# Kernel optimization log

Measured on AMD Instinct MI355X. Metric: run time of the kernel, lower is better.

The kernel has to match this reference:

```python
import jax, jax.numpy as jnp
import numpy as np

BLOCK = 16  # NVFP4 block size (per-block FP8 scale over 16 FP4 values)
FP4_GRID = jnp.array([0.0, 0.5, 1.0, 1.5, 2.0, 3.0, 4.0, 6.0], dtype=jnp.float32)
FP4_MIDS = jnp.array([0.25, 0.75, 1.25, 1.75, 2.5, 3.5, 5.0], dtype=jnp.float32)


def _quantize_fp4(v):
    # round-to-nearest onto the signed E2M1 grid {0,.5,1,1.5,2,3,4,6}
    a = jnp.clip(jnp.abs(v), 0.0, 6.0)
    idx = jnp.searchsorted(FP4_MIDS, a)
    return jnp.sign(v) * FP4_GRID[idx]


def _block_quantize(x):
    # returns (fp4 values, per-16-block scales) such that x ~= q * scale_blocked
    M, K = x.shape
    B = K // BLOCK
    xb = x.reshape(M, B, BLOCK)
    s = jnp.max(jnp.abs(xb), axis=-1) / 6.0 + 1e-8  # [M, B]
    q = _quantize_fp4(xb / s[:, :, None]).reshape(M, K)
    return q, s


def setup_inputs() -> dict:
    key = jax.random.key(0)
    k1, k2, k3 = jax.random.split(key, 3)
    M, K, N = 8192, 4096, 4096
    bsz, q_len = 4, 2048

    x_raw = jax.random.normal(k1, (M, K), dtype=jnp.float32)
    w_raw = jax.random.normal(k2, (N, K), dtype=jnp.float32) * 0.02

    # global weight scale as in NVFP4_reorder_quantize_w: max(w)/(448*6)
    scale_w_global = jnp.max(w_raw) / (448.0 * 6.0)
    qw, scale_w = _block_quantize(w_raw / scale_w_global)

    # activation global scale (produced upstream by the activation quantizer)
    scale_x_global = jnp.max(x_raw) / (448.0 * 6.0)
    qx, scale_x = _block_quantize(x_raw / scale_x_global)

    bias = jax.random.normal(k3, (N,), dtype=jnp.float32) * 0.01

    return {
        "qx": qx,                      # [M, K] FP4-grid values
        "scale_x": scale_x,            # [M, K//16] block scales
        "scale": scale_x_global,       # scalar global activation scale
        "qw": qw,                      # [N, K] FP4-grid values
        "scale_w": scale_w,            # [N, K//16] block scales
        "scale_w_global": scale_w_global,
        "bias": bias,                  # [N]
        "bsz": bsz,
        "q_len": q_len,
    }


def reference(qx, scale_x, scale, qw, scale_w, scale_w_global, bias, bsz, q_len):
    # Dequant-scaled GEMM: y = (qx .* sx)(qw .* sw)^T * (scale * scale_w_global) + bias
    M, K = qx.shape
    N = qw.shape[0]
    B = K // BLOCK
    xd = (qx.reshape(M, B, BLOCK) * scale_x[:, :, None]).reshape(M, K)
    wd = (qw.reshape(N, B, BLOCK) * scale_w[:, :, None]).reshape(N, K)
    y = jnp.einsum("mk,nk->mn", xd, wd) * (scale * scale_w_global)
    y = y + bias
    return y.reshape(bsz, q_len, -1)
```

## Files before the change

kernel.cpp:

```cpp
#include <hip/hip_runtime.h>
#include <cstdint>

#define K_DIM 4096
#define ROWB 13
#define NU   (K_DIM / 32)

typedef __bf16 bf16x8 __attribute__((ext_vector_type(8)));
typedef float f32x4 __attribute__((ext_vector_type(4)));

__device__ inline unsigned short f2bf(float f) {
    union { float f; unsigned int u; } v; v.f = f;
    unsigned int u = v.u;
    return (unsigned short)((u + 0x7FFFu + ((u >> 16) & 1u)) >> 16);
}

__device__ __forceinline__ void gload16(const void* g, void* l) {
    __builtin_amdgcn_global_load_lds(
        (const __attribute__((address_space(1))) unsigned int*)g,
        (__attribute__((address_space(3))) unsigned int*)l,
        16, 0, 0);
}

__global__ __launch_bounds__(256) void dequant2_kernel(
        const float* __restrict__ qx, const float* __restrict__ sx,
        unsigned short* __restrict__ xd, long t8x,
        const float* __restrict__ qw, const float* __restrict__ sw,
        unsigned short* __restrict__ wd, long t8w) {
    long i = (long)blockIdx.x * blockDim.x + threadIdx.x;
    if (i >= t8x + t8w) return;
    const float* q; const float* s; unsigned short* o;
    if (i < t8x) { q = qx; s = sx; o = xd; }
    else         { q = qw; s = sw; o = wd; i -= t8x; }
    long e = i * 8;
    float sc = s[e >> 4];
    float4 v0 = *(const float4*)(q + e);
    float4 v1 = *(const float4*)(q + e + 4);
    union { unsigned short h[8]; uint4 u; } ov;
    ov.h[0] = f2bf(v0.x * sc); ov.h[1] = f2bf(v0.y * sc);
    ov.h[2] = f2bf(v0.z * sc); ov.h[3] = f2bf(v0.w * sc);
    ov.h[4] = f2bf(v1.x * sc); ov.h[5] = f2bf(v1.y * sc);
    ov.h[6] = f2bf(v1.z * sc); ov.h[7] = f2bf(v1.w * sc);
    *(uint4*)(o + e) = ov.u;
}


__global__ __launch_bounds__(512, 2) void gemm256_kernel(
        const unsigned short* __restrict__ A,
        const unsigned short* __restrict__ B,
        const float* __restrict__ sg1, const float* __restrict__ sg2,
        const float* __restrict__ bias,
        float* __restrict__ out, int M, int N) {
    __shared__ __align__(16) char lds[131072];

    const int tid  = threadIdx.x;
    const int lane = tid & 63;
    const int wid  = tid >> 6;
    const int wm   = wid >> 2;
    const int wn   = wid & 3;
    const int l15  = lane & 15;
    const int cb   = (lane >> 4) << 4;
    const int scb  = ((lane & 3) ^ ((lane >> 3) & 3)) << 4;

    const int nbn = N >> 8;
    const int nwg = (M >> 8) * nbn;
    const int cpx = nwg >> 3;
    const int bid = blockIdx.x;
    const int swz = (bid & 7) * cpx + (bid >> 3);
    const int tile_m = (swz / nbn) << 8;
    const int tile_n = (swz % nbn) << 8;

    const int grow = lane >> 2;
    const char* gA0 = (const char*)A +
        ((size_t)(tile_m + 32 * wid + grow) << ROWB) + scb;
    const char* gA1 = gA0 + ((size_t)16 << ROWB);
    const char* gB0 = (const char*)B +
        ((size_t)(tile_n + 32 * wid + grow) << ROWB) + scb;
    const char* gB1 = gB0 + ((size_t)16 << ROWB);
    const int dA0 = wid * 2048;
    const int dB0 = 16384 + wid * 2048;

    const int arow = wm * 128 + l15;
    const int aoff = arow * 64 + (cb ^ (((arow >> 1) & 3) << 4));
    const int brow = wn * 64 + l15;
    const int boff = 16384 + brow * 64 + (cb ^ (((brow >> 1) & 3) << 4));

    f32x4 acc[8][4];
#pragma unroll
    for (int mb = 0; mb < 8; ++mb)
#pragma unroll
        for (int nb = 0; nb < 4; ++nb) acc[mb][nb] = (f32x4){0.f, 0.f, 0.f, 0.f};

#pragma unroll
    for (int pu = 0; pu < 3; ++pu) {
        char* Sb = lds + (pu << 15);
        const int kb = pu << 6;
        gload16(gA0 + kb, Sb + dA0);
        gload16(gA1 + kb, Sb + dA0 + 1024);
        gload16(gB0 + kb, Sb + dB0);
        gload16(gB1 + kb, Sb + dB0 + 1024);
    }
    asm volatile("s_waitcnt vmcnt(8)" ::: "memory");
    __builtin_amdgcn_s_barrier();

    for (int ub = 0; ub < NU; ub += 4) {
#pragma unroll
        for (int uu = 0; uu < 4; ++uu) {
            const int u = ub + uu;
            const char* Ab = lds + (uu << 15);
            char* Sb = lds + (((uu + 3) & 3) << 15);
            const int skb = ((u + 3 < NU) ? (u + 3) : (NU - 1)) << 6;

            bf16x8 bfr[4], afr[4];
#pragma unroll
            for (int nb = 0; nb < 4; ++nb)
                bfr[nb] = *(const bf16x8*)(Ab + boff + nb * 1024);
#pragma unroll
            for (int mb = 0; mb < 4; ++mb)
                afr[mb] = *(const bf16x8*)(Ab + aoff + mb * 1024);
            gload16(gA0 + skb, Sb + dA0);
            gload16(gA1 + skb, Sb + dA0 + 1024);
            __builtin_amdgcn_s_barrier();
            __builtin_amdgcn_s_setprio(1);
#pragma unroll
            for (int mb = 0; mb < 4; ++mb)
#pragma unroll
                for (int nb = 0; nb < 4; ++nb)
                    acc[mb][nb] = __builtin_amdgcn_mfma_f32_16x16x32_bf16(
                        afr[mb], bfr[nb], acc[mb][nb], 0, 0, 0);
            __builtin_amdgcn_s_setprio(0);

            bf16x8 afr2[4];
#pragma unroll
            for (int mb = 0; mb < 4; ++mb)
                afr2[mb] = *(const bf16x8*)(Ab + aoff + 4096 + mb * 1024);
            gload16(gB0 + skb, Sb + dB0);
            gload16(gB1 + skb, Sb + dB0 + 1024);
            __builtin_amdgcn_s_barrier();
            __builtin_amdgcn_s_setprio(1);
#pragma unroll
            for (int mb = 0; mb < 4; ++mb)
#pragma unroll
                for (int nb = 0; nb < 4; ++nb)
                    acc[mb + 4][nb] = __builtin_amdgcn_mfma_f32_16x16x32_bf16(
                        afr2[mb], bfr[nb], acc[mb + 4][nb], 0, 0, 0);
            __builtin_amdgcn_s_setprio(0);

            asm volatile("s_waitcnt vmcnt(8)" ::: "memory");
            __builtin_amdgcn_s_barrier();
        }
    }

    const float gs = sg1[0] * sg2[0];
    const int row0 = tile_m + wm * 128 + ((lane >> 4) << 2);
    const int col0 = tile_n + wn * 64 + l15;
    float bv[4];
#pragma unroll
    for (int nb = 0; nb < 4; ++nb) bv[nb] = bias[col0 + nb * 16];
#pragma unroll
    for (int mb = 0; mb < 8; ++mb)
#pragma unroll
        for (int nb = 0; nb < 4; ++nb) {
            const int col = col0 + nb * 16;
#pragma unroll
            for (int j = 0; j < 4; ++j)
                out[(size_t)(row0 + mb * 16 + j) * N + col] =
                    acc[mb][nb][j] * gs + bv[nb];
        }
}

__global__ __launch_bounds__(256) void gemm_fused_kernel(
        const float* __restrict__ qx, const float* __restrict__ sx,
        const float* __restrict__ qw, const float* __restrict__ sw,
        const float* __restrict__ sg1, const float* __restrict__ sg2,
        const float* __restrict__ bias,
        float* __restrict__ out, int M, int N) {
    __shared__ __align__(16) unsigned short As[128 * 32];
    __shared__ __align__(16) unsigned short Bs[128 * 32];
    const int tid  = threadIdx.x;
    const int lane = tid & 63;
    const int wid  = tid >> 6;
    const int tile_n = blockIdx.x * 128;
    const int tile_m = blockIdx.y * 128;
    const int wm = wid >> 1, wn = wid & 1;
    f32x4 acc[16];
#pragma unroll
    for (int i = 0; i < 16; ++i) acc[i] = (f32x4){0.f, 0.f, 0.f, 0.f};
    const int l15 = lane & 15;
    const int lk  = (lane >> 4) * 8;
    for (int kt = 0; kt < K_DIM / 32; ++kt) {
#pragma unroll
        for (int cc = 0; cc < 2; ++cc) {
            const int c   = tid + cc * 256;
            const int row = c >> 2;
            const int col = (c & 3) * 8;
            const int gk  = kt * 32 + col;
            {
                const float* qp = qx + (long)(tile_m + row) * K_DIM + gk;
                float s = sx[(long)(tile_m + row) * (K_DIM / 16) + (gk >> 4)];
                float4 a0 = *(const float4*)qp;
                float4 a1 = *(const float4*)(qp + 4);
                union { unsigned short h[8]; uint4 u; } o;
                o.h[0] = f2bf(a0.x * s); o.h[1] = f2bf(a0.y * s);
                o.h[2] = f2bf(a0.z * s); o.h[3] = f2bf(a0.w * s);
                o.h[4] = f2bf(a1.x * s); o.h[5] = f2bf(a1.y * s);
                o.h[6] = f2bf(a1.z * s); o.h[7] = f2bf(a1.w * s);
                *(uint4*)&As[row * 32 + col] = o.u;
            }
            {
                const float* qp = qw + (long)(tile_n + row) * K_DIM + gk;
                float s = sw[(long)(tile_n + row) * (K_DIM / 16) + (gk >> 4)];
                float4 a0 = *(const float4*)qp;
                float4 a1 = *(const float4*)(qp + 4);
                union { unsigned short h[8]; uint4 u; } o;
                o.h[0] = f2bf(a0.x * s); o.h[1] = f2bf(a0.y * s);
                o.h[2] = f2bf(a0.z * s); o.h[3] = f2bf(a0.w * s);
                o.h[4] = f2bf(a1.x * s); o.h[5] = f2bf(a1.y * s);
                o.h[6] = f2bf(a1.z * s); o.h[7] = f2bf(a1.w * s);
                *(uint4*)&Bs[row * 32 + col] = o.u;
            }
        }
        __syncthreads();
        const unsigned short* pa = As + (wm * 64 + l15) * 32 + lk;
        const unsigned short* pb = Bs + (wn * 64 + l15) * 32 + lk;
        bf16x8 a[4], b[4];
#pragma unroll
        for (int i = 0; i < 4; ++i) {
            a[i] = *(const bf16x8*)(pa + i * 16 * 32);
            b[i] = *(const bf16x8*)(pb + i * 16 * 32);
        }
#pragma unroll
        for (int mi = 0; mi < 4; ++mi)
#pragma unroll
            for (int ni = 0; ni < 4; ++ni)
                acc[mi * 4 + ni] = __builtin_amdgcn_mfma_f32_16x16x32_bf16(
                    a[mi], b[ni], acc[mi * 4 + ni], 0, 0, 0);
        __syncthreads();
    }
    const float gs = sg1[0] * sg2[0];
    const int row0 = tile_m + wm * 64 + (lane >> 4) * 4;
    const int col0 = tile_n + wn * 64 + l15;
#pragma unroll
    for (int mi = 0; mi < 4; ++mi)
#pragma unroll
        for (int ni = 0; ni < 4; ++ni) {
            const int col = col0 + ni * 16;
            const float bv = bias[col];
#pragma unroll
            for (int j = 0; j < 4; ++j)
                out[(long)(row0 + mi * 16 + j) * N + col] =
                    acc[mi * 4 + ni][j] * gs + bv;
        }
}

extern "C" void kernel_launch(void* const* d_in, const int* in_sizes, int n_in,
                              void* d_out, int out_size, void* d_ws, size_t ws_size,
                              hipStream_t stream) {
    const float* qx   = (const float*)d_in[0];
    const float* sx   = (const float*)d_in[1];
    const float* sc   = (const float*)d_in[2];
    const float* qw   = (const float*)d_in[3];
    const float* sw   = (const float*)d_in[4];
    const float* swg  = (const float*)d_in[5];
    const float* bias = (const float*)d_in[6];
    float* out = (float*)d_out;

    const int M = in_sizes[0] / K_DIM;
    const int N = in_sizes[3] / K_DIM;

    const size_t needA = (size_t)M * K_DIM * sizeof(unsigned short);
    const size_t needB = (size_t)N * K_DIM * sizeof(unsigned short);

    if (ws_size >= needA + needB) {
        unsigned short* xd = (unsigned short*)d_ws;
        unsigned short* wd = (unsigned short*)((char*)d_ws + needA);
        long t8x = (long)M * K_DIM / 8;
        long t8w = (long)N * K_DIM / 8;
        long tot = t8x + t8w;
        dequant2_kernel<<<(int)((tot + 255) / 256), 256, 0, stream>>>(
            qx, sx, xd, t8x, qw, sw, wd, t8w);
        const int nwg = (M / 256) * (N / 256);
        gemm256_kernel<<<nwg, 512, 0, stream>>>(xd, wd, sc, swg, bias, out, M, N);
    } else {
        dim3 grid(N / 128, M / 128);
        gemm_fused_kernel<<<grid, 256, 0, stream>>>(
            qx, sx, qw, sw, sc, swg, bias, out, M, N);
    }
}
```

Measured before the change: 283.8 us.

## Switch GEMM inner loop to 32x32x16 bf16 MFMA and drop mid-iteration barriers

```diff
diff --git a/kernel.cpp b/kernel.cpp
--- a/kernel.cpp
+++ b/kernel.cpp
@@ -6,7 +6,8 @@
 #define NU   (K_DIM / 32)
 
 typedef __bf16 bf16x8 __attribute__((ext_vector_type(8)));
-typedef float f32x4 __attribute__((ext_vector_type(4)));
+typedef float f32x4  __attribute__((ext_vector_type(4)));
+typedef float f32x16 __attribute__((ext_vector_type(16)));
 
 __device__ inline unsigned short f2bf(float f) {
     union { float f; unsigned int u; } v; v.f = f;
@@ -57,8 +58,8 @@
     const int wid  = tid >> 6;
     const int wm   = wid >> 2;
     const int wn   = wid & 3;
-    const int l15  = lane & 15;
-    const int cb   = (lane >> 4) << 4;
+    const int l31  = lane & 31;
+    const int lhi  = lane >> 5;
     const int scb  = ((lane & 3) ^ ((lane >> 3) & 3)) << 4;
 
     const int nbn = N >> 8;
@@ -79,16 +80,22 @@
     const int dA0 = wid * 2048;
     const int dB0 = 16384 + wid * 2048;
 
-    const int arow = wm * 128 + l15;
-    const int aoff = arow * 64 + (cb ^ (((arow >> 1) & 3) << 4));
-    const int brow = wn * 64 + l15;
-    const int boff = 16384 + brow * 64 + (cb ^ (((brow >> 1) & 3) << 4));
-
-    f32x4 acc[8][4];
-#pragma unroll
-    for (int mb = 0; mb < 8; ++mb)
-#pragma unroll
-        for (int nb = 0; nb < 4; ++nb) acc[mb][nb] = (f32x4){0.f, 0.f, 0.f, 0.f};
+    const int arow = wm * 128 + l31;
+    const int axv  = (arow >> 1) & 3;
+    const int aok0 = arow * 64 + ((lhi ^ axv) << 4);
+    const int aok1 = arow * 64 + (((2 + lhi) ^ axv) << 4);
+    const int brow = wn * 64 + l31;
+    const int bxv  = (brow >> 1) & 3;
+    const int bok0 = 16384 + brow * 64 + ((lhi ^ bxv) << 4);
+    const int bok1 = 16384 + brow * 64 + (((2 + lhi) ^ bxv) << 4);
+
+    f32x16 acc[4][2];
+#pragma unroll
+    for (int mb = 0; mb < 4; ++mb)
+#pragma unroll
+        for (int nb = 0; nb < 2; ++nb)
+#pragma unroll
+            for (int j = 0; j < 16; ++j) acc[mb][nb][j] = 0.f;
 
 #pragma unroll
     for (int pu = 0; pu < 3; ++pu) {
@@ -105,44 +112,37 @@
     for (int ub = 0; ub < NU; ub += 4) {
 #pragma unroll
         for (int uu = 0; uu < 4; ++uu) {
-            const int u = ub + uu;
-            const char* Ab = lds + (uu << 15);
+            const int u  = ub + uu;
+            const char* Sl = lds + (uu << 15);
             char* Sb = lds + (((uu + 3) & 3) << 15);
             const int skb = ((u + 3 < NU) ? (u + 3) : (NU - 1)) << 6;
 
-            bf16x8 bfr[4], afr[4];
-#pragma unroll
-            for (int nb = 0; nb < 4; ++nb)
-                bfr[nb] = *(const bf16x8*)(Ab + boff + nb * 1024);
-#pragma unroll
-            for (int mb = 0; mb < 4; ++mb)
-                afr[mb] = *(const bf16x8*)(Ab + aoff + mb * 1024);
             gload16(gA0 + skb, Sb + dA0);
             gload16(gA1 + skb, Sb + dA0 + 1024);
-            __builtin_amdgcn_s_barrier();
-            __builtin_amdgcn_s_setprio(1);
-#pragma unroll
-            for (int mb = 0; mb < 4; ++mb)
-#pragma unroll
-                for (int nb = 0; nb < 4; ++nb)
-                    acc[mb][nb] = __builtin_amdgcn_mfma_f32_16x16x32_bf16(
-                        afr[mb], bfr[nb], acc[mb][nb], 0, 0, 0);
-            __builtin_amdgcn_s_setprio(0);
-
-            bf16x8 afr2[4];
-#pragma unroll
-            for (int mb = 0; mb < 4; ++mb)
-                afr2[mb] = *(const bf16x8*)(Ab + aoff + 4096 + mb * 1024);
             gload16(gB0 + skb, Sb + dB0);
             gload16(gB1 + skb, Sb + dB0 + 1024);
-            __builtin_amdgcn_s_barrier();
+
+            bf16x8 af[4][2], bf[2][2];
+#pragma unroll
+            for (int nb = 0; nb < 2; ++nb) {
+                bf[nb][0] = *(const bf16x8*)(Sl + bok0 + nb * 2048);
+                bf[nb][1] = *(const bf16x8*)(Sl + bok1 + nb * 2048);
+            }
+#pragma unroll
+            for (int mb = 0; mb < 4; ++mb) {
+                af[mb][0] = *(const bf16x8*)(Sl + aok0 + mb * 2048);
+                af[mb][1] = *(const bf16x8*)(Sl + aok1 + mb * 2048);
+            }
+
             __builtin_amdgcn_s_setprio(1);
 #pragma unroll
             for (int mb = 0; mb < 4; ++mb)
 #pragma unroll
-                for (int nb = 0; nb < 4; ++nb)
-                    acc[mb + 4][nb] = __builtin_amdgcn_mfma_f32_16x16x32_bf16(
-                        afr2[mb], bfr[nb], acc[mb + 4][nb], 0, 0, 0);
+                for (int nb = 0; nb < 2; ++nb)
+#pragma unroll
+                    for (int ks = 0; ks < 2; ++ks)
+                        acc[mb][nb] = __builtin_amdgcn_mfma_f32_32x32x16_bf16(
+                            af[mb][ks], bf[nb][ks], acc[mb][nb], 0, 0, 0);
             __builtin_amdgcn_s_setprio(0);
 
             asm volatile("s_waitcnt vmcnt(8)" ::: "memory");
@@ -151,20 +151,23 @@
     }
 
     const float gs = sg1[0] * sg2[0];
-    const int row0 = tile_m + wm * 128 + ((lane >> 4) << 2);
-    const int col0 = tile_n + wn * 64 + l15;
-    float bv[4];
-#pragma unroll
-    for (int nb = 0; nb < 4; ++nb) bv[nb] = bias[col0 + nb * 16];
-#pragma unroll
-    for (int mb = 0; mb < 8; ++mb)
-#pragma unroll
-        for (int nb = 0; nb < 4; ++nb) {
-            const int col = col0 + nb * 16;
-#pragma unroll
-            for (int j = 0; j < 4; ++j)
-                out[(size_t)(row0 + mb * 16 + j) * N + col] =
-                    acc[mb][nb][j] * gs + bv[nb];
+    const int row0 = tile_m + wm * 128 + 4 * lhi;
+    const int col0 = tile_n + wn * 64 + l31;
+    float bv[2];
+#pragma unroll
+    for (int nb = 0; nb < 2; ++nb) bv[nb] = bias[col0 + nb * 32];
+#pragma unroll
+    for (int mb = 0; mb < 4; ++mb)
+#pragma unroll
+        for (int nb = 0; nb < 2; ++nb) {
+            const int col = col0 + nb * 32;
+#pragma unroll
+            for (int g = 0; g < 4; ++g)
+#pragma unroll
+                for (int r = 0; r < 4; ++r) {
+                    const int row = row0 + mb * 32 + 8 * g + r;
+                    out[(size_t)row * N + col] = acc[mb][nb][g * 4 + r] * gs + bv[nb];
+                }
         }
 }
 
```

New measurement: 322.2 us. 13.5% more time.

## Register double-buffer LDS fragments to overlap LDS reads with MFMA

Applied to the files above, without the earlier changes.

```diff
diff --git a/kernel.cpp b/kernel.cpp
--- a/kernel.cpp
+++ b/kernel.cpp
@@ -72,10 +72,8 @@
     const int grow = lane >> 2;
     const char* gA0 = (const char*)A +
         ((size_t)(tile_m + 32 * wid + grow) << ROWB) + scb;
-    const char* gA1 = gA0 + ((size_t)16 << ROWB);
     const char* gB0 = (const char*)B +
         ((size_t)(tile_n + 32 * wid + grow) << ROWB) + scb;
-    const char* gB1 = gB0 + ((size_t)16 << ROWB);
     const int dA0 = wid * 2048;
     const int dB0 = 16384 + wid * 2048;
 
@@ -90,64 +88,82 @@
 #pragma unroll
         for (int nb = 0; nb < 4; ++nb) acc[mb][nb] = (f32x4){0.f, 0.f, 0.f, 0.f};
 
+    bf16x8 a0f[8], b0f[4], a1f[8], b1f[4];
+
 #pragma unroll
     for (int pu = 0; pu < 3; ++pu) {
         char* Sb = lds + (pu << 15);
         const int kb = pu << 6;
         gload16(gA0 + kb, Sb + dA0);
-        gload16(gA1 + kb, Sb + dA0 + 1024);
+        gload16(gA0 + kb + ((size_t)16 << ROWB), Sb + dA0 + 1024);
         gload16(gB0 + kb, Sb + dB0);
-        gload16(gB1 + kb, Sb + dB0 + 1024);
+        gload16(gB0 + kb + ((size_t)16 << ROWB), Sb + dB0 + 1024);
     }
     asm volatile("s_waitcnt vmcnt(8)" ::: "memory");
     __builtin_amdgcn_s_barrier();
-
-    for (int ub = 0; ub < NU; ub += 4) {
-#pragma unroll
-        for (int uu = 0; uu < 4; ++uu) {
-            const int u = ub + uu;
-            const char* Ab = lds + (uu << 15);
-            char* Sb = lds + (((uu + 3) & 3) << 15);
-            const int skb = ((u + 3 < NU) ? (u + 3) : (NU - 1)) << 6;
-
-            bf16x8 bfr[4], afr[4];
+#pragma unroll
+    for (int nb = 0; nb < 4; ++nb) b0f[nb] = *(const bf16x8*)(lds + boff + nb * 1024);
+#pragma unroll
+    for (int mb = 0; mb < 8; ++mb) a0f[mb] = *(const bf16x8*)(lds + aoff + mb * 1024);
+
+    for (int b = 0; b < NU; b += 2) {
+        asm volatile("s_waitcnt vmcnt(4)" ::: "memory");
+        __builtin_amdgcn_s_barrier();
+        {
+            const int sku = (b + 3 < NU) ? (b + 3) : (NU - 1);
+            char* Sb = lds + (((b + 3) & 3) << 15);
+            const int skb = sku << 6;
+            gload16(gA0 + skb, Sb + dA0);
+            gload16(gA0 + skb + ((size_t)16 << ROWB), Sb + dA0 + 1024);
+            gload16(gB0 + skb, Sb + dB0);
+            gload16(gB0 + skb + ((size_t)16 << ROWB), Sb + dB0 + 1024);
+        }
+        {
+            const char* Sr = lds + (((b + 1) & 3) << 15);
 #pragma unroll
             for (int nb = 0; nb < 4; ++nb)
-                bfr[nb] = *(const bf16x8*)(Ab + boff + nb * 1024);
-#pragma unroll
-            for (int mb = 0; mb < 4; ++mb)
-                afr[mb] = *(const bf16x8*)(Ab + aoff + mb * 1024);
+                b1f[nb] = *(const bf16x8*)(Sr + boff + nb * 1024);
+#pragma unroll
+            for (int mb = 0; mb < 8; ++mb)
+                a1f[mb] = *(const bf16x8*)(Sr + aoff + mb * 1024);
+        }
+        __builtin_amdgcn_s_setprio(1);
+#pragma unroll
+        for (int mb = 0; mb < 8; ++mb)
+#pragma unroll
+            for (int nb = 0; nb < 4; ++nb)
+                acc[mb][nb] = __builtin_amdgcn_mfma_f32_16x16x32_bf16(
+                    a0f[mb], b0f[nb], acc[mb][nb], 0, 0, 0);
+        __builtin_amdgcn_s_setprio(0);
+
+        asm volatile("s_waitcnt vmcnt(4)" ::: "memory");
+        __builtin_amdgcn_s_barrier();
+        {
+            const int sku = (b + 4 < NU) ? (b + 4) : (NU - 1);
+            char* Sb = lds + (((b + 4) & 3) << 15);
+            const int skb = sku << 6;
             gload16(gA0 + skb, Sb + dA0);
-            gload16(gA1 + skb, Sb + dA0 + 1024);
-            __builtin_amdgcn_s_barrier();
-            __builtin_amdgcn_s_setprio(1);
-#pragma unroll
-            for (int mb = 0; mb < 4; ++mb)
-#pragma unroll
-                for (int nb = 0; nb < 4; ++nb)
-                    acc[mb][nb] = __builtin_amdgcn_mfma_f32_16x16x32_bf16(
-                        afr[mb], bfr[nb], acc[mb][nb], 0, 0, 0);
-            __builtin_amdgcn_s_setprio(0);
-
-            bf16x8 afr2[4];
-#pragma unroll
-            for (int mb = 0; mb < 4; ++mb)
-                afr2[mb] = *(const bf16x8*)(Ab + aoff + 4096 + mb * 1024);
+            gload16(gA0 + skb + ((size_t)16 << ROWB), Sb + dA0 + 1024);
             gload16(gB0 + skb, Sb + dB0);
-            gload16(gB1 + skb, Sb + dB0 + 1024);
-            __builtin_amdgcn_s_barrier();
-            __builtin_amdgcn_s_setprio(1);
-#pragma unroll
-            for (int mb = 0; mb < 4; ++mb)
-#pragma unroll
-                for (int nb = 0; nb < 4; ++nb)
-                    acc[mb + 4][nb] = __builtin_amdgcn_mfma_f32_16x16x32_bf16(
-                        afr2[mb], bfr[nb], acc[mb + 4][nb], 0, 0, 0);
-            __builtin_amdgcn_s_setprio(0);
-
-            asm volatile("s_waitcnt vmcnt(8)" ::: "memory");
-            __builtin_amdgcn_s_barrier();
-        }
+            gload16(gB0 + skb + ((size_t)16 << ROWB), Sb + dB0 + 1024);
+        }
+        {
+            const char* Sr = lds + (((b + 2) & 3) << 15);
+#pragma unroll
+            for (int nb = 0; nb < 4; ++nb)
+                b0f[nb] = *(const bf16x8*)(Sr + boff + nb * 1024);
+#pragma unroll
+            for (int mb = 0; mb < 8; ++mb)
+                a0f[mb] = *(const bf16x8*)(Sr + aoff + mb * 1024);
+        }
+        __builtin_amdgcn_s_setprio(1);
+#pragma unroll
+        for (int mb = 0; mb < 8; ++mb)
+#pragma unroll
+            for (int nb = 0; nb < 4; ++nb)
+                acc[mb][nb] = __builtin_amdgcn_mfma_f32_16x16x32_bf16(
+                    a1f[mb], b1f[nb], acc[mb][nb], 0, 0, 0);
+        __builtin_amdgcn_s_setprio(0);
     }
 
     const float gs = sg1[0] * sg2[0];
```

Result: slower. 291.0 us (+2.6%).

## Switch GEMM to 128x256 tiles with 4 waves and 3-stage LDS ring

Applied to the files above, without the earlier changes.

```diff
diff --git a/kernel.cpp b/kernel.cpp
--- a/kernel.cpp
+++ b/kernel.cpp
@@ -44,45 +44,40 @@
 }
 
 
-__global__ __launch_bounds__(512, 2) void gemm256_kernel(
+__global__ __launch_bounds__(256, 2) void gemm128x256_kernel(
         const unsigned short* __restrict__ A,
         const unsigned short* __restrict__ B,
         const float* __restrict__ sg1, const float* __restrict__ sg2,
         const float* __restrict__ bias,
         float* __restrict__ out, int M, int N) {
-    __shared__ __align__(16) char lds[131072];
+    __shared__ __align__(16) char lds[73728];
 
     const int tid  = threadIdx.x;
     const int lane = tid & 63;
     const int wid  = tid >> 6;
-    const int wm   = wid >> 2;
-    const int wn   = wid & 3;
     const int l15  = lane & 15;
     const int cb   = (lane >> 4) << 4;
     const int scb  = ((lane & 3) ^ ((lane >> 3) & 3)) << 4;
 
     const int nbn = N >> 8;
-    const int nwg = (M >> 8) * nbn;
+    const int nwg = (M >> 7) * nbn;
     const int cpx = nwg >> 3;
     const int bid = blockIdx.x;
     const int swz = (bid & 7) * cpx + (bid >> 3);
-    const int tile_m = (swz / nbn) << 8;
+    const int tile_m = (swz / nbn) << 7;
     const int tile_n = (swz % nbn) << 8;
 
     const int grow = lane >> 2;
     const char* gA0 = (const char*)A +
         ((size_t)(tile_m + 32 * wid + grow) << ROWB) + scb;
-    const char* gA1 = gA0 + ((size_t)16 << ROWB);
     const char* gB0 = (const char*)B +
-        ((size_t)(tile_n + 32 * wid + grow) << ROWB) + scb;
-    const char* gB1 = gB0 + ((size_t)16 << ROWB);
+        ((size_t)(tile_n + 64 * wid + grow) << ROWB) + scb;
     const int dA0 = wid * 2048;
-    const int dB0 = 16384 + wid * 2048;
-
-    const int arow = wm * 128 + l15;
-    const int aoff = arow * 64 + (cb ^ (((arow >> 1) & 3) << 4));
-    const int brow = wn * 64 + l15;
-    const int boff = 16384 + brow * 64 + (cb ^ (((brow >> 1) & 3) << 4));
+    const int dB0 = 8192 + wid * 4096;
+
+    const int aoff = l15 * 64 + (cb ^ (((l15 >> 1) & 3) << 4));
+    const int brow = wid * 64 + l15;
+    const int boff = 8192 + brow * 64 + (cb ^ (((brow >> 1) & 3) << 4));
 
     f32x4 acc[8][4];
 #pragma unroll
@@ -91,68 +86,71 @@
         for (int nb = 0; nb < 4; ++nb) acc[mb][nb] = (f32x4){0.f, 0.f, 0.f, 0.f};
 
 #pragma unroll
-    for (int pu = 0; pu < 3; ++pu) {
-        char* Sb = lds + (pu << 15);
+    for (int pu = 0; pu < 2; ++pu) {
+        char* Sb = lds + pu * 24576;
         const int kb = pu << 6;
         gload16(gA0 + kb, Sb + dA0);
-        gload16(gA1 + kb, Sb + dA0 + 1024);
+        gload16(gA0 + kb + ((size_t)16 << ROWB), Sb + dA0 + 1024);
         gload16(gB0 + kb, Sb + dB0);
-        gload16(gB1 + kb, Sb + dB0 + 1024);
-    }
-    asm volatile("s_waitcnt vmcnt(8)" ::: "memory");
+        gload16(gB0 + kb + ((size_t)16 << ROWB), Sb + dB0 + 1024);
+        gload16(gB0 + kb + ((size_t)32 << ROWB), Sb + dB0 + 2048);
+        gload16(gB0 + kb + ((size_t)48 << ROWB), Sb + dB0 + 3072);
+    }
+    asm volatile("s_waitcnt vmcnt(6)" ::: "memory");
     __builtin_amdgcn_s_barrier();
 
-    for (int ub = 0; ub < NU; ub += 4) {
-#pragma unroll
-        for (int uu = 0; uu < 4; ++uu) {
-            const int u = ub + uu;
-            const char* Ab = lds + (uu << 15);
-            char* Sb = lds + (((uu + 3) & 3) << 15);
-            const int skb = ((u + 3 < NU) ? (u + 3) : (NU - 1)) << 6;
-
-            bf16x8 bfr[4], afr[4];
-#pragma unroll
-            for (int nb = 0; nb < 4; ++nb)
-                bfr[nb] = *(const bf16x8*)(Ab + boff + nb * 1024);
-#pragma unroll
-            for (int mb = 0; mb < 4; ++mb)
-                afr[mb] = *(const bf16x8*)(Ab + aoff + mb * 1024);
-            gload16(gA0 + skb, Sb + dA0);
-            gload16(gA1 + skb, Sb + dA0 + 1024);
-            __builtin_amdgcn_s_barrier();
-            __builtin_amdgcn_s_setprio(1);
-#pragma unroll
-            for (int mb = 0; mb < 4; ++mb)
-#pragma unroll
-                for (int nb = 0; nb < 4; ++nb)
-                    acc[mb][nb] = __builtin_amdgcn_mfma_f32_16x16x32_bf16(
-                        afr[mb], bfr[nb], acc[mb][nb], 0, 0, 0);
-            __builtin_amdgcn_s_setprio(0);
-
-            bf16x8 afr2[4];
-#pragma unroll
-            for (int mb = 0; mb < 4; ++mb)
-                afr2[mb] = *(const bf16x8*)(Ab + aoff + 4096 + mb * 1024);
-            gload16(gB0 + skb, Sb + dB0);
-            gload16(gB1 + skb, Sb + dB0 + 1024);
-            __builtin_amdgcn_s_barrier();
-            __builtin_amdgcn_s_setprio(1);
-#pragma unroll
-            for (int mb = 0; mb < 4; ++mb)
-#pragma unroll
-                for (int nb = 0; nb < 4; ++nb)
-                    acc[mb + 4][nb] = __builtin_amdgcn_mfma_f32_16x16x32_bf16(
-                        afr2[mb], bfr[nb], acc[mb + 4][nb], 0, 0, 0);
-            __builtin_amdgcn_s_setprio(0);
-
-            asm volatile("s_waitcnt vmcnt(8)" ::: "memory");
-            __builtin_amdgcn_s_barrier();
-        }
-    }
+#define UNIT_BODY(SKU, CUR, STG) do {                                        \
+    const int skb = (SKU) << 6;                                              \
+    bf16x8 bfr[4], afr[4], afr2[4];                                          \
+    _Pragma("unroll")                                                        \
+    for (int nb = 0; nb < 4; ++nb)                                           \
+        bfr[nb] = *(const bf16x8*)(lds + (CUR) + boff + nb * 1024);          \
+    _Pragma("unroll")                                                        \
+    for (int mb = 0; mb < 4; ++mb)                                           \
+        afr[mb] = *(const bf16x8*)(lds + (CUR) + aoff + mb * 1024);          \
+    gload16(gA0 + skb, lds + (STG) + dA0);                                   \
+    gload16(gA0 + skb + ((size_t)16 << ROWB), lds + (STG) + dA0 + 1024);     \
+    gload16(gB0 + skb, lds + (STG) + dB0);                                   \
+    __builtin_amdgcn_s_barrier();                                            \
+    __builtin_amdgcn_s_setprio(1);                                           \
+    _Pragma("unroll")                                                        \
+    for (int mb = 0; mb < 4; ++mb)                                           \
+        _Pragma("unroll")                                                    \
+        for (int nb = 0; nb < 4; ++nb)                                       \
+            acc[mb][nb] = __builtin_amdgcn_mfma_f32_16x16x32_bf16(           \
+                afr[mb], bfr[nb], acc[mb][nb], 0, 0, 0);                     \
+    __builtin_amdgcn_s_setprio(0);                                           \
+    _Pragma("unroll")                                                        \
+    for (int mb = 0; mb < 4; ++mb)                                           \
+        afr2[mb] = *(const bf16x8*)(lds + (CUR) + aoff + 4096 + mb * 1024);  \
+    gload16(gB0 + skb + ((size_t)16 << ROWB), lds + (STG) + dB0 + 1024);     \
+    gload16(gB0 + skb + ((size_t)32 << ROWB), lds + (STG) + dB0 + 2048);     \
+    gload16(gB0 + skb + ((size_t)48 << ROWB), lds + (STG) + dB0 + 3072);     \
+    __builtin_amdgcn_s_barrier();                                            \
+    __builtin_amdgcn_s_setprio(1);                                           \
+    _Pragma("unroll")                                                        \
+    for (int mb = 0; mb < 4; ++mb)                                           \
+        _Pragma("unroll")                                                    \
+        for (int nb = 0; nb < 4; ++nb)                                       \
+            acc[mb + 4][nb] = __builtin_amdgcn_mfma_f32_16x16x32_bf16(       \
+                afr2[mb], bfr[nb], acc[mb + 4][nb], 0, 0, 0);                \
+    __builtin_amdgcn_s_setprio(0);                                           \
+    asm volatile("s_waitcnt vmcnt(6)" ::: "memory");                         \
+    __builtin_amdgcn_s_barrier();                                            \
+} while (0)
+
+    for (int ub = 0; ub < 126; ub += 3) {
+        UNIT_BODY(ub + 2, 0,     49152);
+        UNIT_BODY(ub + 3, 24576, 0);
+        UNIT_BODY(ub + 4, 49152, 24576);
+    }
+    UNIT_BODY(127, 0,     49152);
+    UNIT_BODY(127, 24576, 0);
+#undef UNIT_BODY
 
     const float gs = sg1[0] * sg2[0];
-    const int row0 = tile_m + wm * 128 + ((lane >> 4) << 2);
-    const int col0 = tile_n + wn * 64 + l15;
+    const int row0 = tile_m + ((lane >> 4) << 2);
+    const int col0 = tile_n + wid * 64 + l15;
     float bv[4];
 #pragma unroll
     for (int nb = 0; nb < 4; ++nb) bv[nb] = bias[col0 + nb * 16];
@@ -278,8 +276,8 @@
         long tot = t8x + t8w;
         dequant2_kernel<<<(int)((tot + 255) / 256), 256, 0, stream>>>(
             qx, sx, xd, t8x, qw, sw, wd, t8w);
-        const int nwg = (M / 256) * (N / 256);
-        gemm256_kernel<<<nwg, 512, 0, stream>>>(xd, wd, sc, swg, bias, out, M, N);
+        const int nwg = (M / 128) * (N / 256);
+        gemm128x256_kernel<<<nwg, 256, 0, stream>>>(xd, wd, sc, swg, bias, out, M, N);
     } else {
         dim3 grid(N / 128, M / 128);
         gemm_fused_kernel<<<grid, 256, 0, stream>>>(
```

Result: slower. 323.3 us (+13.9%).
